# Optimization experiments

Measured on AMD Instinct MI355X. Metric: run time of the kernel, lower is better.

## Reference

```python
import jax, jax.numpy as jnp
import numpy as np

EMBED = 1024
NHEAD = 16
HEAD_DIM = EMBED // NHEAD
DFF = 4096
TOP_K = 64
LN_EPS = 1e-5


def _layernorm(x, g, b):
    mu = jnp.mean(x, axis=-1, keepdims=True)
    var = jnp.var(x, axis=-1, keepdims=True)
    return (x - mu) * jax.lax.rsqrt(var + LN_EPS) * g + b


def setup_inputs() -> dict:
    key = jax.random.key(0)
    ks = jax.random.split(key, 12)
    s = 0.02
    return {
        "x": jax.random.normal(ks[0], (2, 2048, EMBED), dtype=jnp.float32),
        "Wq": jax.random.normal(ks[1], (EMBED, EMBED), dtype=jnp.float32) * s,
        "bq": jnp.zeros((EMBED,), jnp.float32),
        "Wk": jax.random.normal(ks[2], (EMBED, EMBED), dtype=jnp.float32) * s,
        "bk": jnp.zeros((EMBED,), jnp.float32),
        "Wv": jax.random.normal(ks[3], (EMBED, EMBED), dtype=jnp.float32) * s,
        "bv": jnp.zeros((EMBED,), jnp.float32),
        "Wo": jax.random.normal(ks[4], (EMBED, EMBED), dtype=jnp.float32) * s,
        "bo": jnp.zeros((EMBED,), jnp.float32),
        "g1": jnp.ones((EMBED,), jnp.float32),
        "be1": jnp.zeros((EMBED,), jnp.float32),
        "g2": jnp.ones((EMBED,), jnp.float32),
        "be2": jnp.zeros((EMBED,), jnp.float32),
        "W1": jax.random.normal(ks[5], (EMBED, DFF), dtype=jnp.float32) * s,
        "b1": jnp.zeros((DFF,), jnp.float32),
        "W2": jax.random.normal(ks[6], (DFF, EMBED), dtype=jnp.float32) * s,
        "b2": jnp.zeros((EMBED,), jnp.float32),
    }


def reference(x, Wq, bq, Wk, bk, Wv, bv, Wo, bo, g1, be1, g2, be2, W1, b1, W2, b2):
    B, N, E = x.shape
    res = x
    h = _layernorm(x, g1, be1)
    # [B, H, N, D]
    q = (h @ Wq + bq).reshape(B, N, NHEAD, HEAD_DIM).transpose(0, 2, 1, 3)
    k = (h @ Wk + bk).reshape(B, N, NHEAD, HEAD_DIM).transpose(0, 2, 1, 3)
    v = (h @ Wv + bv).reshape(B, N, NHEAD, HEAD_DIM).transpose(0, 2, 1, 3)
    scores = jnp.einsum("bhqd,bhkd->bhqk", q, k) / jnp.sqrt(jnp.float32(HEAD_DIM))
    if TOP_K < N:
        topv, _ = jax.lax.top_k(scores, TOP_K)  # [B,H,N,TOP_K]
        thresh = topv[..., -1:, ]
        scores = jnp.where(scores < thresh, -jnp.inf, scores)
    attn = jax.nn.softmax(scores, axis=-1)
    out = jnp.einsum("bhqk,bhkd->bhqd", attn, v)
    out = out.transpose(0, 2, 1, 3).reshape(B, N, E)
    out = out @ Wo + bo
    x1 = res + out  # dropout is identity at eval
    h2 = _layernorm(x1, g2, be2)
    ff = jax.nn.gelu(h2 @ W1 + b1, approximate=False) @ W2 + b2
    return x1 + ff
```

## Files before the change

### kernel.cpp

```cpp
#include <hip/hip_runtime.h>

typedef short short8v __attribute__((ext_vector_type(8)));
typedef float floatx4 __attribute__((ext_vector_type(4)));
typedef unsigned short us4 __attribute__((ext_vector_type(4)));
typedef unsigned short us2 __attribute__((ext_vector_type(2)));

#define EMB 1024
#define QKVW 3072
#define SEQ 2048
#define NH 16
#define HD 64
#define TOPK 64
#define QBLK 16
#define CAP 128
#define SROW 2056
#define QSCALE 0.18033688f
#define ATTN_SMEM (QBLK * SROW * 2 + QBLK * CAP * 4)

#define GLDS16(gp, lp)                                                        \
  __builtin_amdgcn_global_load_lds(                                           \
      (const __attribute__((address_space(1))) void*)(gp),                    \
      (__attribute__((address_space(3))) void*)(lp), 16, 0, 0)

#if __has_builtin(__builtin_amdgcn_exp2f)
#define EXP2F(x) __builtin_amdgcn_exp2f(x)
#else
#define EXP2F(x) exp2f(x)
#endif

static __device__ __forceinline__ unsigned short f2b(float f) {
  union { float f; unsigned u; } in; in.f = f;
  unsigned u = in.u;
  return (unsigned short)((u + 0x7FFFu + ((u >> 16) & 1u)) >> 16);
}
static __device__ __forceinline__ float b2f(unsigned short b) {
  union { unsigned u; float f; } o; o.u = ((unsigned)b) << 16;
  return o.f;
}
static __device__ __forceinline__ unsigned mmap(unsigned s) {
  return (s & 0x8000u) ? (~s & 0xFFFFu) : (s | 0x8000u);
}
static __device__ __forceinline__ unsigned short munmap(unsigned u) {
  return (u & 0x8000u) ? (unsigned short)(u ^ 0x8000u) : (unsigned short)(~u & 0xFFFFu);
}

__global__ __launch_bounds__(256) void ln_kernel(const float* __restrict__ X,
    const float* __restrict__ gam, const float* __restrict__ bet,
    unsigned short* __restrict__ H) {
  const int row = blockIdx.x;
  const int tid = threadIdx.x;
  const float4 v = *(const float4*)&X[(size_t)row * EMB + tid * 4];
  float s1 = v.x + v.y + v.z + v.w;
  float s2 = v.x * v.x + v.y * v.y + v.z * v.z + v.w * v.w;
#pragma unroll
  for (int off = 32; off; off >>= 1) { s1 += __shfl_xor(s1, off); s2 += __shfl_xor(s2, off); }
  __shared__ float red[2][4];
  const int w = tid >> 6, l = tid & 63;
  if (l == 0) { red[0][w] = s1; red[1][w] = s2; }
  __syncthreads();
  s1 = red[0][0] + red[0][1] + red[0][2] + red[0][3];
  s2 = red[1][0] + red[1][1] + red[1][2] + red[1][3];
  const float mu = s1 * (1.f / EMB);
  const float var = s2 * (1.f / EMB) - mu * mu;
  const float rs = rsqrtf(var + 1e-5f);
  const float4 gv = *(const float4*)&gam[tid * 4];
  const float4 bv = *(const float4*)&bet[tid * 4];
  us4 o;
  o.x = f2b((v.x - mu) * rs * gv.x + bv.x);
  o.y = f2b((v.y - mu) * rs * gv.y + bv.y);
  o.z = f2b((v.z - mu) * rs * gv.z + bv.z);
  o.w = f2b((v.w - mu) * rs * gv.w + bv.w);
  *(us4*)&H[(size_t)row * EMB + tid * 4] = o;
}

__global__ __launch_bounds__(256) void wcvt_all_kernel(
    const float* __restrict__ Wq, const float* __restrict__ Wk,
    const float* __restrict__ Wv, const float* __restrict__ Wo,
    const float* __restrict__ W1, const float* __restrict__ W2,
    const float* __restrict__ bq, const float* __restrict__ bk,
    const float* __restrict__ bv,
    unsigned short* __restrict__ WqkvT, unsigned short* __restrict__ WoT,
    unsigned short* __restrict__ W1T, unsigned short* __restrict__ W2T,
    float* __restrict__ bqkv) {
  const int bid = blockIdx.x;
  const int tid = threadIdx.x;
  if (bid >= 3072) {
    const int i = (bid - 3072) * 256 + tid;
    float v;
    if (i < 1024) v = bq[i] * QSCALE;
    else if (i < 2048) v = bk[i - 1024];
    else v = bv[i - 2048];
    bqkv[i] = v;
    return;
  }
  const float* W; unsigned short* WT; int K, N, t; float scale = 1.f;
  if (bid < 768) {
    const int seg = bid >> 8; t = bid & 255;
    W = (seg == 0) ? Wq : ((seg == 1) ? Wk : Wv);
    WT = WqkvT + (size_t)seg * 1024 * 1024;
    K = 1024; N = 1024;
    if (seg == 0) scale = QSCALE;
  } else if (bid < 1024) {
    t = bid - 768;  W = Wo; WT = WoT; K = 1024; N = 1024;
  } else if (bid < 2048) {
    t = bid - 1024; W = W1; WT = W1T; K = 1024; N = 4096;
  } else {
    t = bid - 2048; W = W2; WT = W2T; K = 4096; N = 1024;
  }
  const int sh = (N == 4096) ? 6 : 4;
  const int n0 = (t & ((1 << sh) - 1)) * 64, k0 = (t >> sh) * 64;
  __shared__ unsigned short tl[64][72];
#pragma unroll
  for (int i = 0; i < 4; ++i) {
    const int f = i * 256 + tid;
    const int k = f >> 4, n4 = (f & 15) * 4;
    const float4 v = *(const float4*)&W[(size_t)(k0 + k) * N + n0 + n4];
    tl[n4 + 0][k] = f2b(v.x * scale);
    tl[n4 + 1][k] = f2b(v.y * scale);
    tl[n4 + 2][k] = f2b(v.z * scale);
    tl[n4 + 3][k] = f2b(v.w * scale);
  }
  __syncthreads();
#pragma unroll
  for (int i = 0; i < 2; ++i) {
    const int f = i * 256 + tid;
    const int n = f >> 3, c8 = (f & 7) * 8;
    short8v o;
#pragma unroll
    for (int j = 0; j < 8; ++j) o[j] = (short)tl[n][c8 + j];
    *(short8v*)&WT[(size_t)(n0 + n) * K + k0 + c8] = o;
  }
}

static __device__ __forceinline__ void xcd_tile(int& bm, int& bn, int tn) {
  const int gx = gridDim.x;
  const int nwg = gx * gridDim.y;
  const int flat = blockIdx.y * gx + blockIdx.x;
  const int q8 = nwg >> 3;
  const int wg = (flat & 7) * q8 + (flat >> 3);
  bm = (wg / gx) * 128;
  bn = (wg % gx) * tn;
}

template <int EPI>
__global__ __launch_bounds__(256) void gemm_bt4_kernel(
    const unsigned short* __restrict__ A, const unsigned short* __restrict__ BT,
    const float* __restrict__ bias, const float* __restrict__ res,
    void* __restrict__ Cout, int M, int N, int K) {
  __shared__ __align__(16) unsigned short lA[128 * 32];
  __shared__ __align__(16) unsigned short lB[128 * 32];
  const int tid = threadIdx.x;
  const int l = tid & 63, w = tid >> 6;
  const int wm = (w >> 1) * 64, wn = (w & 1) * 64;
  int bm, bn; xcd_tile(bm, bn, 128);
  const int g = l >> 4, r16 = l & 15;
  const int lr = l >> 2, lc = (l & 3) * 8;
  floatx4 acc[4][4] = {};
  for (int kt = 0; kt < K; kt += 32) {
#pragma unroll
    for (int j = 0; j < 2; ++j) {
      GLDS16(&A[(size_t)(bm + w * 32 + j * 16 + lr) * K + kt + lc],
             &lA[(w * 32 + j * 16) * 32]);
      GLDS16(&BT[(size_t)(bn + w * 32 + j * 16 + lr) * K + kt + lc],
             &lB[(w * 32 + j * 16) * 32]);
    }
    __syncthreads();
    short8v a[4], b[4];
#pragma unroll
    for (int m = 0; m < 4; ++m) a[m] = *(const short8v*)&lA[(wm + m * 16 + r16) * 32 + g * 8];
#pragma unroll
    for (int n = 0; n < 4; ++n) b[n] = *(const short8v*)&lB[(wn + n * 16 + r16) * 32 + g * 8];
#pragma unroll
    for (int m = 0; m < 4; ++m)
#pragma unroll
      for (int n = 0; n < 4; ++n)
        acc[m][n] = __builtin_amdgcn_mfma_f32_16x16x32_bf16(a[m], b[n], acc[m][n], 0, 0, 0);
    __syncthreads();
  }
#pragma unroll
  for (int m = 0; m < 4; ++m) {
#pragma unroll
    for (int n = 0; n < 4; ++n) {
#pragma unroll
      for (int r = 0; r < 4; ++r) {
        const int gm = bm + wm + m * 16 + g * 4 + r;
        const int gn = bn + wn + n * 16 + r16;
        float v = acc[m][n][r] + bias[gn];
        if constexpr (EPI == 0) {
          ((unsigned short*)Cout)[(size_t)gm * N + gn] = f2b(v);
        } else if constexpr (EPI == 1) {
          const float ge = 0.5f * v * (1.f + erff(v * 0.70710678118f));
          ((unsigned short*)Cout)[(size_t)gm * N + gn] = f2b(ge);
        } else {
          ((float*)Cout)[(size_t)gm * N + gn] = v + res[(size_t)gm * N + gn];
        }
      }
    }
  }
}

template <int EPI>
__global__ __launch_bounds__(256) void gemm_n64_kernel(
    const unsigned short* __restrict__ A, const unsigned short* __restrict__ BT,
    const float* __restrict__ bias, const float* __restrict__ res,
    void* __restrict__ Cout, int M, int N, int K) {
  __shared__ __align__(16) unsigned short lA[128 * 32];
  __shared__ __align__(16) unsigned short lB[64 * 32];
  const int tid = threadIdx.x;
  const int l = tid & 63, w = tid >> 6;
  const int wm = (w & 1) * 64, wn = (w >> 1) * 32;
  int bm, bn; xcd_tile(bm, bn, 64);
  const int g = l >> 4, r16 = l & 15;
  const int lr = l >> 2, lc = (l & 3) * 8;
  floatx4 acc[4][2] = {};
  for (int kt = 0; kt < K; kt += 32) {
#pragma unroll
    for (int j = 0; j < 2; ++j)
      GLDS16(&A[(size_t)(bm + w * 32 + j * 16 + lr) * K + kt + lc],
             &lA[(w * 32 + j * 16) * 32]);
    GLDS16(&BT[(size_t)(bn + w * 16 + lr) * K + kt + lc], &lB[(w * 16) * 32]);
    __syncthreads();
    short8v a[4], b[2];
#pragma unroll
    for (int m = 0; m < 4; ++m) a[m] = *(const short8v*)&lA[(wm + m * 16 + r16) * 32 + g * 8];
#pragma unroll
    for (int n = 0; n < 2; ++n) b[n] = *(const short8v*)&lB[(wn + n * 16 + r16) * 32 + g * 8];
#pragma unroll
    for (int m = 0; m < 4; ++m)
#pragma unroll
      for (int n = 0; n < 2; ++n)
        acc[m][n] = __builtin_amdgcn_mfma_f32_16x16x32_bf16(a[m], b[n], acc[m][n], 0, 0, 0);
    __syncthreads();
  }
#pragma unroll
  for (int m = 0; m < 4; ++m) {
#pragma unroll
    for (int n = 0; n < 2; ++n) {
#pragma unroll
      for (int r = 0; r < 4; ++r) {
        const int gm = bm + wm + m * 16 + g * 4 + r;
        const int gn = bn + wn + n * 16 + r16;
        float v = acc[m][n][r] + bias[gn];
        if constexpr (EPI == 0) {
          ((unsigned short*)Cout)[(size_t)gm * N + gn] = f2b(v);
        } else if constexpr (EPI == 1) {
          const float ge = 0.5f * v * (1.f + erff(v * 0.70710678118f));
          ((unsigned short*)Cout)[(size_t)gm * N + gn] = f2b(ge);
        } else {
          ((float*)Cout)[(size_t)gm * N + gn] = v + res[(size_t)gm * N + gn];
        }
      }
    }
  }
}

__global__ __launch_bounds__(1024, 8) void attn_kernel(
    const unsigned short* __restrict__ qkv, unsigned short* __restrict__ O) {
  extern __shared__ unsigned short smem[];
  unsigned short (*scores)[SROW] = (unsigned short(*)[SROW])smem;
  unsigned* hist = (unsigned*)(smem + QBLK * SROW);

  const int tid = threadIdx.x;
  const int l = tid & 63, w = tid >> 6;
  const int g = l >> 4, r16 = l & 15;
  const int qb = blockIdx.x;
  const int h = blockIdx.y;
  const int bz = blockIdx.z;
  const size_t rowbase = (size_t)bz * SEQ;
  const int hcol = h * HD;

  ((uint2*)hist)[tid] = uint2{0u, 0u};

  {
    const size_t qrow = (rowbase + qb * QBLK + r16) * QKVW + hcol;
    const short8v a0 = *(const short8v*)&qkv[qrow + g * 8];
    const short8v a1 = *(const short8v*)&qkv[qrow + 32 + g * 8];
    const int kbase = w * 128;
#pragma unroll 2
    for (int kti = 0; kti < 8; ++kti) {
      const int key0 = kbase + kti * 16;
      const size_t krow = (rowbase + key0 + r16) * QKVW + 1024 + hcol;
      const short8v b0 = *(const short8v*)&qkv[krow + g * 8];
      const short8v b1 = *(const short8v*)&qkv[krow + 32 + g * 8];
      floatx4 acc = {0.f, 0.f, 0.f, 0.f};
      acc = __builtin_amdgcn_mfma_f32_16x16x32_bf16(a0, b0, acc, 0, 0, 0);
      acc = __builtin_amdgcn_mfma_f32_16x16x32_bf16(a1, b1, acc, 0, 0, 0);
#pragma unroll
      for (int r = 0; r < 4; ++r) {
        union { float f; unsigned u; } cv; cv.f = acc[r];
        scores[g * 4 + r][key0 + r16] = (unsigned short)mmap(cv.u >> 16);
      }
    }
  }
  __syncthreads();

  const unsigned long long ltmask = (1ull << l) - 1ull;
  const int quarter = l >> 4, j16 = l & 15;
  const int q = w;
  unsigned* srow32 = (unsigned*)&scores[q][0];
  unsigned* comp = &hist[q * CAP];

  unsigned ux[16];
  us2 mx2 = {0, 0};
#pragma unroll
  for (int i = 0; i < 16; ++i) {
    const unsigned x = srow32[l + 64 * i];
    ux[i] = x;
    union { unsigned u; us2 v; } c; c.u = x;
    mx2 = __builtin_elementwise_max(mx2, c.v);
  }
  unsigned um = (mx2.x > mx2.y) ? (unsigned)mx2.x : (unsigned)mx2.y;
#pragma unroll
  for (int off = 32; off; off >>= 1) {
    const unsigned o2 = (unsigned)__shfl_xor((int)um, off);
    um = (o2 > um) ? o2 : um;
  }
  const float mf = b2f(munmap(um));

#pragma unroll
  for (int i = 0; i < 16; ++i) {
    const unsigned d0 = um - (ux[i] & 0xFFFFu);
    const unsigned d1 = um - (ux[i] >> 16);
    if (d0 < 256u) atomicAdd(&comp[d0 >> 1], 1u << ((d0 & 1u) * 16));
    if (d1 < 256u) atomicAdd(&comp[d1 >> 1], 1u << ((d1 & 1u) * 16));
  }
  asm volatile("s_waitcnt lgkmcnt(0)" ::: "memory");
  unsigned ut;
  {
    const unsigned w0 = comp[2 * l], w1 = comp[2 * l + 1];
    const unsigned c0 = w0 & 0xFFFFu, c1 = w0 >> 16, c2 = w1 & 0xFFFFu, c3 = w1 >> 16;
    const unsigned s4 = c0 + c1 + c2 + c3;
    unsigned incl = s4;
#pragma unroll
    for (int off = 1; off < 64; off <<= 1) {
      const unsigned t2 = (unsigned)__shfl_up((int)incl, off);
      if (l >= off) incl += t2;
    }
    const unsigned pre = incl - s4;
    unsigned dc = 0xFFFFFFFFu;
    if      (pre + c0 >= TOPK)           dc = 4 * l;
    else if (pre + c0 + c1 >= TOPK)      dc = 4 * l + 1;
    else if (pre + c0 + c1 + c2 >= TOPK) dc = 4 * l + 2;
    else if (incl >= TOPK)               dc = 4 * l + 3;
#pragma unroll
    for (int off = 32; off; off >>= 1) {
      const unsigned o2 = (unsigned)__shfl_xor((int)dc, off);
      dc = (o2 < dc) ? o2 : dc;
    }
    if (dc != 0xFFFFFFFFu) {
      ut = um - dc;
    } else {
      unsigned t = 0;
#pragma unroll 1
      for (int bit = 15; bit >= 0; --bit) {
        const unsigned cand = t | (1u << bit);
        int c = 0;
#pragma unroll
        for (int i = 0; i < 16; ++i) {
          c += __popcll(__ballot((ux[i] & 0xFFFFu) >= cand));
          c += __popcll(__ballot((ux[i] >> 16) >= cand));
        }
        if (c >= TOPK) t = cand;
      }
      ut = t;
    }
  }

  unsigned base = 0;
#pragma unroll
  for (int i = 0; i < 16; ++i) {
    const unsigned u0 = ux[i] & 0xFFFFu, u1 = ux[i] >> 16;
    const bool k0 = (u0 >= ut), k1 = (u1 >= ut);
    const unsigned key0 = 2 * (l + 64 * i);
    const unsigned long long m0 = __ballot(k0);
    if (k0) {
      const unsigned pos = base + (unsigned)__popcll(m0 & ltmask);
      if (pos < CAP) comp[pos] = (key0 << 16) | u0;
    }
    base += (unsigned)__popcll(m0);
    const unsigned long long m1 = __ballot(k1);
    if (k1) {
      const unsigned pos = base + (unsigned)__popcll(m1 & ltmask);
      if (pos < CAP) comp[pos] = ((key0 + 1) << 16) | u1;
    }
    base += (unsigned)__popcll(m1);
  }
  const unsigned cnt = (base < CAP) ? base : CAP;

  float e0 = 0.f, e1 = 0.f;
  unsigned c0v = 0, c1v = 0;
  const bool h0 = ((unsigned)l < cnt), h1 = ((unsigned)(l + 64) < cnt);
  if (h0) {
    c0v = comp[l];
    e0 = EXP2F(b2f(munmap(c0v & 0xFFFFu)) - mf);
  }
  if (h1) {
    c1v = comp[l + 64];
    e1 = EXP2F(b2f(munmap(c1v & 0xFFFFu)) - mf);
  }
  float lsum = e0 + e1;
#pragma unroll
  for (int off = 32; off; off >>= 1) lsum += __shfl_xor(lsum, off);
  const float rinv = 1.f / lsum;
  if (h0) {
    unsigned pp; asm("v_cvt_pk_bf16_f32 %0, %1, %2" : "=v"(pp) : "v"(e0), "v"(e0));
    comp[l] = (c0v & 0xFFFF0000u) | (pp & 0xFFFFu);
  }
  if (h1) {
    unsigned pp; asm("v_cvt_pk_bf16_f32 %0, %1, %2" : "=v"(pp) : "v"(e1), "v"(e1));
    comp[l + 64] = (c1v & 0xFFFF0000u) | (pp & 0xFFFFu);
  }

  const unsigned short* vbase = &qkv[rowbase * QKVW + 2048 + hcol + j16 * 4];
  float a0 = 0.f, a1 = 0.f, a2 = 0.f, a3 = 0.f;
#pragma unroll 4
  for (int k = 0; k < 16; ++k) {
    const unsigned c = comp[k * 4 + quarter];
    const float p = b2f((unsigned short)(c & 0xFFFFu));
    const unsigned idx = c >> 16;
    const uint2 vv = *(const uint2*)&vbase[(size_t)idx * QKVW];
    union { unsigned u; float f; } t0, t1, t2, t3;
    t0.u = vv.x << 16; t1.u = vv.x & 0xFFFF0000u;
    t2.u = vv.y << 16; t3.u = vv.y & 0xFFFF0000u;
    a0 += p * t0.f; a1 += p * t1.f; a2 += p * t2.f; a3 += p * t3.f;
  }
#pragma unroll 1
  for (unsigned k = 64; k < cnt; k += 4) {
    const unsigned kk = k + quarter;
    const unsigned c = (kk < cnt) ? comp[kk] : 0u;
    const float p = b2f((unsigned short)(c & 0xFFFFu));
    const unsigned idx = c >> 16;
    const uint2 vv = *(const uint2*)&vbase[(size_t)idx * QKVW];
    union { unsigned u; float f; } t0, t1, t2, t3;
    t0.u = vv.x << 16; t1.u = vv.x & 0xFFFF0000u;
    t2.u = vv.y << 16; t3.u = vv.y & 0xFFFF0000u;
    a0 += p * t0.f; a1 += p * t1.f; a2 += p * t2.f; a3 += p * t3.f;
  }
  a0 += __shfl_xor(a0, 16); a0 += __shfl_xor(a0, 32);
  a1 += __shfl_xor(a1, 16); a1 += __shfl_xor(a1, 32);
  a2 += __shfl_xor(a2, 16); a2 += __shfl_xor(a2, 32);
  a3 += __shfl_xor(a3, 16); a3 += __shfl_xor(a3, 32);
  if (l < 16) {
    unsigned w0, w1;
    const float r0 = a0 * rinv, r1 = a1 * rinv, r2 = a2 * rinv, r3 = a3 * rinv;
    asm("v_cvt_pk_bf16_f32 %0, %1, %2" : "=v"(w0) : "v"(r0), "v"(r1));
    asm("v_cvt_pk_bf16_f32 %0, %1, %2" : "=v"(w1) : "v"(r2), "v"(r3));
    uint2 ow; ow.x = w0; ow.y = w1;
    *(uint2*)&O[(rowbase + qb * QBLK + q) * EMB + hcol + j16 * 4] = ow;
  }
}

extern "C" void kernel_launch(void* const* d_in, const int* in_sizes, int n_in,
                              void* d_out, int out_size, void* d_ws, size_t ws_size,
                              hipStream_t stream) {
  (void)in_sizes; (void)n_in; (void)out_size; (void)ws_size;
  const float* x  = (const float*)d_in[0];
  const float* Wq = (const float*)d_in[1];
  const float* bq = (const float*)d_in[2];
  const float* Wk = (const float*)d_in[3];
  const float* bk = (const float*)d_in[4];
  const float* Wv = (const float*)d_in[5];
  const float* bv = (const float*)d_in[6];
  const float* Wo = (const float*)d_in[7];
  const float* bo = (const float*)d_in[8];
  const float* g1 = (const float*)d_in[9];
  const float* be1 = (const float*)d_in[10];
  const float* g2 = (const float*)d_in[11];
  const float* be2 = (const float*)d_in[12];
  const float* W1 = (const float*)d_in[13];
  const float* b1 = (const float*)d_in[14];
  const float* W2 = (const float*)d_in[15];
  const float* b2 = (const float*)d_in[16];
  float* out = (float*)d_out;

  char* ws = (char*)d_ws;
  float* x1 = (float*)ws;
  unsigned short* hbuf  = (unsigned short*)(ws + ((size_t)16 << 20));
  unsigned short* qkvb  = (unsigned short*)(ws + ((size_t)24 << 20));
  unsigned short* Ob    = (unsigned short*)(ws + ((size_t)48 << 20));
  unsigned short* ff1   = (unsigned short*)(ws + ((size_t)24 << 20));
  float* bqkv           = (float*)(ws + ((size_t)48 << 20));
  unsigned short* WqkvT = (unsigned short*)(ws + ((size_t)56 << 20));
  unsigned short* WoT   = (unsigned short*)(ws + ((size_t)62 << 20));
  unsigned short* W1T   = (unsigned short*)(ws + ((size_t)64 << 20));
  unsigned short* W2T   = (unsigned short*)(ws + ((size_t)72 << 20));

  wcvt_all_kernel<<<dim3(3084), 256, 0, stream>>>(Wq, Wk, Wv, Wo, W1, W2, bq, bk, bv,
                                                  WqkvT, WoT, W1T, W2T, bqkv);

  ln_kernel<<<dim3(4096), 256, 0, stream>>>(x, g1, be1, hbuf);
  gemm_bt4_kernel<0><<<dim3(24, 32), 256, 0, stream>>>(hbuf, WqkvT, bqkv, nullptr, qkvb,
                                                       4096, QKVW, 1024);
  (void)hipFuncSetAttribute((const void*)attn_kernel,
                            hipFuncAttributeMaxDynamicSharedMemorySize, ATTN_SMEM);
  attn_kernel<<<dim3(128, 16, 2), 1024, ATTN_SMEM, stream>>>(qkvb, Ob);
  gemm_n64_kernel<2><<<dim3(16, 32), 256, 0, stream>>>(Ob, WoT, bo, x, x1, 4096, 1024, 1024);
  ln_kernel<<<dim3(4096), 256, 0, stream>>>(x1, g2, be2, hbuf);
  gemm_bt4_kernel<1><<<dim3(32, 32), 256, 0, stream>>>(hbuf, W1T, b1, nullptr, ff1,
                                                       4096, 4096, 1024);
  gemm_n64_kernel<2><<<dim3(16, 32), 256, 0, stream>>>(ff1, W2T, b2, x1, out, 4096, 1024, 4096);
}
```

Measured before the change: 401.6 us.

## Deepen GEMM K-tile to 64 with XOR-swizzled LDS and vectorize score stores

The bf16 GEMM now stages a 64-wide K slice per iteration instead of 32, with an XOR swizzle on LDS columns so that the wider rows avoid bank conflicts. This halves the number of barrier pairs per K loop at the cost of doubling LDS per block. In the attention score phase the MFMA operands are swapped so each lane holds four consecutive keys. The four bf16 order-mapped scores are packed with perm and a paired mmap and written in a single 8-byte LDS store, replacing four scalar 2-byte stores.

```diff
diff --git a/kernel.cpp b/kernel.cpp
--- a/kernel.cpp
+++ b/kernel.cpp
@@ -42,6 +42,10 @@
 }
 static __device__ __forceinline__ unsigned short munmap(unsigned u) {
   return (u & 0x8000u) ? (unsigned short)(u ^ 0x8000u) : (unsigned short)(~u & 0xFFFFu);
+}
+static __device__ __forceinline__ unsigned mmap2(unsigned s) {
+  const unsigned t = ((s >> 15) & 0x00010001u) * 0x7FFFu;
+  return s ^ (0x80008000u | t);
 }
 
 __global__ __launch_bounds__(256) void ln_kernel(const float* __restrict__ X,
@@ -147,34 +151,40 @@
     const unsigned short* __restrict__ A, const unsigned short* __restrict__ BT,
     const float* __restrict__ bias, const float* __restrict__ res,
     void* __restrict__ Cout, int M, int N, int K) {
-  __shared__ __align__(16) unsigned short lA[128 * 32];
-  __shared__ __align__(16) unsigned short lB[128 * 32];
+  __shared__ __align__(16) unsigned short lA[128 * 64];
+  __shared__ __align__(16) unsigned short lB[128 * 64];
   const int tid = threadIdx.x;
   const int l = tid & 63, w = tid >> 6;
   const int wm = (w >> 1) * 64, wn = (w & 1) * 64;
   int bm, bn; xcd_tile(bm, bn, 128);
   const int g = l >> 4, r16 = l & 15;
-  const int lr = l >> 2, lc = (l & 3) * 8;
+  const int lr8 = l >> 3;
+  const int lc8s = (((l & 7) ^ (lr8 & 7)) * 8);
+  const int xr = (r16 & 7) * 8;
   floatx4 acc[4][4] = {};
-  for (int kt = 0; kt < K; kt += 32) {
-#pragma unroll
-    for (int j = 0; j < 2; ++j) {
-      GLDS16(&A[(size_t)(bm + w * 32 + j * 16 + lr) * K + kt + lc],
-             &lA[(w * 32 + j * 16) * 32]);
-      GLDS16(&BT[(size_t)(bn + w * 32 + j * 16 + lr) * K + kt + lc],
-             &lB[(w * 32 + j * 16) * 32]);
+  for (int kt = 0; kt < K; kt += 64) {
+#pragma unroll
+    for (int j = 0; j < 4; ++j) {
+      GLDS16(&A[(size_t)(bm + w * 32 + j * 8 + lr8) * K + kt + lc8s],
+             &lA[(w * 32 + j * 8) * 64]);
+      GLDS16(&BT[(size_t)(bn + w * 32 + j * 8 + lr8) * K + kt + lc8s],
+             &lB[(w * 32 + j * 8) * 64]);
     }
     __syncthreads();
-    short8v a[4], b[4];
-#pragma unroll
-    for (int m = 0; m < 4; ++m) a[m] = *(const short8v*)&lA[(wm + m * 16 + r16) * 32 + g * 8];
-#pragma unroll
-    for (int n = 0; n < 4; ++n) b[n] = *(const short8v*)&lB[(wn + n * 16 + r16) * 32 + g * 8];
-#pragma unroll
-    for (int m = 0; m < 4; ++m)
-#pragma unroll
-      for (int n = 0; n < 4; ++n)
-        acc[m][n] = __builtin_amdgcn_mfma_f32_16x16x32_bf16(a[m], b[n], acc[m][n], 0, 0, 0);
+#pragma unroll
+    for (int kk = 0; kk < 2; ++kk) {
+      short8v a[4], b[4];
+      const int co = (kk * 32 + g * 8) ^ xr;
+#pragma unroll
+      for (int m = 0; m < 4; ++m) a[m] = *(const short8v*)&lA[(wm + m * 16 + r16) * 64 + co];
+#pragma unroll
+      for (int n = 0; n < 4; ++n) b[n] = *(const short8v*)&lB[(wn + n * 16 + r16) * 64 + co];
+#pragma unroll
+      for (int m = 0; m < 4; ++m)
+#pragma unroll
+        for (int n = 0; n < 4; ++n)
+          acc[m][n] = __builtin_amdgcn_mfma_f32_16x16x32_bf16(a[m], b[n], acc[m][n], 0, 0, 0);
+    }
     __syncthreads();
   }
 #pragma unroll
@@ -273,23 +283,24 @@
 
   {
     const size_t qrow = (rowbase + qb * QBLK + r16) * QKVW + hcol;
-    const short8v a0 = *(const short8v*)&qkv[qrow + g * 8];
-    const short8v a1 = *(const short8v*)&qkv[qrow + 32 + g * 8];
+    const short8v qf0 = *(const short8v*)&qkv[qrow + g * 8];
+    const short8v qf1 = *(const short8v*)&qkv[qrow + 32 + g * 8];
     const int kbase = w * 128;
 #pragma unroll 2
     for (int kti = 0; kti < 8; ++kti) {
       const int key0 = kbase + kti * 16;
       const size_t krow = (rowbase + key0 + r16) * QKVW + 1024 + hcol;
-      const short8v b0 = *(const short8v*)&qkv[krow + g * 8];
-      const short8v b1 = *(const short8v*)&qkv[krow + 32 + g * 8];
+      const short8v kf0 = *(const short8v*)&qkv[krow + g * 8];
+      const short8v kf1 = *(const short8v*)&qkv[krow + 32 + g * 8];
       floatx4 acc = {0.f, 0.f, 0.f, 0.f};
-      acc = __builtin_amdgcn_mfma_f32_16x16x32_bf16(a0, b0, acc, 0, 0, 0);
-      acc = __builtin_amdgcn_mfma_f32_16x16x32_bf16(a1, b1, acc, 0, 0, 0);
-#pragma unroll
-      for (int r = 0; r < 4; ++r) {
-        union { float f; unsigned u; } cv; cv.f = acc[r];
-        scores[g * 4 + r][key0 + r16] = (unsigned short)mmap(cv.u >> 16);
-      }
+      acc = __builtin_amdgcn_mfma_f32_16x16x32_bf16(kf0, qf0, acc, 0, 0, 0);
+      acc = __builtin_amdgcn_mfma_f32_16x16x32_bf16(kf1, qf1, acc, 0, 0, 0);
+      union { float f; unsigned u; } c0, c1, c2, c3;
+      c0.f = acc[0]; c1.f = acc[1]; c2.f = acc[2]; c3.f = acc[3];
+      const unsigned p01 = __builtin_amdgcn_perm(c1.u, c0.u, 0x07060302u);
+      const unsigned p23 = __builtin_amdgcn_perm(c3.u, c2.u, 0x07060302u);
+      uint2 pw; pw.x = mmap2(p01); pw.y = mmap2(p23);
+      *(uint2*)&scores[r16][key0 + g * 4] = pw;
     }
   }
   __syncthreads();
```

Result: no change. 398.4 us (-0.8%).
